# Performance work log

Hardware: AMD Instinct MI355X
Metric: run time of the kernel (lower is better)

## Reference

```python
import jax, jax.numpy as jnp
import numpy as np

EPS = 1e-8

def setup_inputs() -> dict:
    key = jax.random.key(0)
    kq, kk, kc, ks = jax.random.split(key, 4)
    d, m, K, Q, N = 128, 128, 4, 512, 131072
    query = jax.random.normal(kq, (Q, d), jnp.float32)
    keys = jax.random.normal(kk, (N, d), jnp.float32)
    # per-coordinate MSE codebook centers (sorted), scaled for unit-norm vectors in R^d
    codebook = jnp.sort(jax.random.normal(kc, (K,), jnp.float32)) / jnp.sqrt(jnp.float32(d))
    # QJL random projection matrix S: (m, d)
    S = jax.random.normal(ks, (m, d), jnp.float32)
    return {"query": query, "keys": keys, "codebook": codebook, "S": S}

def reference(query, keys, codebook, S):
    m = S.shape[0]
    # --- quantize(keys): Algorithm 2 ---
    vec_norm = jnp.linalg.norm(keys, axis=-1)                    # (N,)  ||x||
    x_norm = keys / (vec_norm[:, None] + EPS)                    # normalize
    # Stage 1: MSE codebook quantize (per-coordinate nearest center)
    idx = jnp.argmin(jnp.abs(x_norm[..., None] - codebook), axis=-1)  # (N, d)
    x_mse = codebook[idx]                                        # dequantize (gather)
    # residual
    r = x_norm - x_mse                                           # (N, d)
    r_norm = jnp.linalg.norm(r, axis=-1)                         # (N,)
    # Stage 2: QJL sign quantization of projected residual
    signs = jnp.where(r @ S.T >= 0, 1.0, -1.0).astype(keys.dtype)  # (N, m)
    # --- inner_product(query, compressed) ---
    term1 = query @ x_mse.T                                      # (Q, N)  <q, k_mse>
    Sq = query @ S.T                                             # (Q, m)
    scale = jnp.sqrt(jnp.pi / 2.0) / m
    term2 = (Sq @ signs.T) * (r_norm * scale)[None, :]           # QJL correction
    return (term1 + term2) * vec_norm[None, :]                   # rescale by ||k||
```

## Files before the change

kernel.cpp:

```cpp
#include <hip/hip_runtime.h>
#include <stdint.h>


typedef __attribute__((ext_vector_type(8))) short bf16x8;
typedef __attribute__((ext_vector_type(4))) float f32x4;

__device__ __forceinline__ uint16_t f2bf(float x) {
    uint32_t u = __builtin_bit_cast(uint32_t, x);
    uint32_t r = (u + 0x7fffu + ((u >> 16) & 1u)) >> 16;
    return (uint16_t)r;
}

__device__ __forceinline__ void load_lds16(const void* g, void* l) {
    __builtin_amdgcn_global_load_lds(
        (const __attribute__((address_space(1))) void*)g,
        (__attribute__((address_space(3))) void*)l, 16, 0, 0);
}

#define SLD 129

__global__ __launch_bounds__(256) void prep_keys(
    const float* __restrict__ keys, const float* __restrict__ codebook,
    const float* __restrict__ S, uint16_t* __restrict__ Bhat, int N)
{
    __shared__ float S_lds[128 * SLD];
    __shared__ float r_rm[16 * 132];
    __shared__ float rtmp[128];
    __shared__ float vn_sh[16];
    __shared__ float w_sh[16];

    const int tid = threadIdx.x;
    const int lane = tid & 63;
    const float c0 = codebook[0], c1 = codebook[1], c2 = codebook[2], c3 = codebook[3];
    const float scale = 0.009791516697777346f;

    for (int f = tid; f < 4096; f += 256) {
        float4 v = ((const float4*)S)[f];
        int j = f >> 5;
        int i0 = (f & 31) * 4;
        float* p = &S_lds[j * SLD + i0];
        p[0] = v.x; p[1] = v.y; p[2] = v.z; p[3] = v.w;
    }

    for (int tile = 0; tile < 16; ++tile) {
        const int n0 = blockIdx.x * 256 + tile * 16;
        __syncthreads();

        #pragma unroll
        for (int u = 0; u < 2; ++u) {
            int f = u * 256 + tid;
            int row = f >> 5;
            int i0 = (f & 31) * 4;
            float4 v = ((const float4*)(keys + (size_t)(n0 + row) * 128))[f & 31];
            *(float4*)&r_rm[row * 132 + i0] = v;
        }
        __syncthreads();

        if (tid < 128) {
            int row = tid >> 3, k = tid & 7;
            const float* x = &r_rm[row * 132];
            float a;
            {
                #pragma clang fp contract(off)
                float x0 = x[k];
                a = x0 * x0;
                for (int t = 1; t < 16; ++t) {
                    float xv = x[t * 8 + k];
                    a = a + xv * xv;
                }
            }
            rtmp[tid] = a;
        }
        __syncthreads();

        if (tid < 16) {
            const float* r = &rtmp[tid * 8];
            float res = ((r[0] + r[1]) + (r[2] + r[3])) + ((r[4] + r[5]) + (r[6] + r[7]));
            vn_sh[tid] = sqrtf(res);
        }
        __syncthreads();

        {
            int row = tid >> 4, i0 = (tid & 15) * 8;
            float vn = vn_sh[row];
            float denom = vn + 1e-8f;
            float rsq = 0.f;
            uint32_t pk[4];
            float rloc[8];
            #pragma unroll
            for (int u = 0; u < 8; ++u) {
                float xv = r_rm[row * 132 + i0 + u];
                float xn = xv / denom;
                float b = c0, d = fabsf(xn - c0), t;
                t = fabsf(xn - c1); if (t < d) { d = t; b = c1; }
                t = fabsf(xn - c2); if (t < d) { d = t; b = c2; }
                t = fabsf(xn - c3); if (t < d) { d = t; b = c3; }
                float rv = xn - b;
                rloc[u] = rv;
                rsq += rv * rv;
                uint32_t bv = f2bf(vn * b);
                if (u & 1) pk[u >> 1] |= bv << 16; else pk[u >> 1] = bv;
            }
            *(uint4*)(Bhat + (size_t)(n0 + row) * 256 + i0) = *(uint4*)pk;
            *(float4*)&r_rm[row * 132 + i0] = *(float4*)&rloc[0];
            *(float4*)&r_rm[row * 132 + i0 + 4] = *(float4*)&rloc[4];
            #pragma unroll
            for (int off2 = 1; off2 < 16; off2 <<= 1) rsq += __shfl_xor(rsq, off2);
            if ((tid & 15) == 0) w_sh[row] = sqrtf(rsq) * scale * vn;
        }
        __syncthreads();

        {
            const int rowgrp = tid >> 7;
            const int j = tid & 127;
            float rr[8][2];
            #pragma unroll
            for (int k = 0; k < 8; ++k) {
                rr[k][0] = r_rm[(rowgrp * 8 + k) * 132 + lane];
                rr[k][1] = r_rm[(rowgrp * 8 + k) * 132 + 64 + lane];
            }
            float acc[8] = {0.f, 0.f, 0.f, 0.f, 0.f, 0.f, 0.f, 0.f};
            const float* Sj = &S_lds[j * SLD];
            #pragma unroll
            for (int h = 0; h < 2; ++h) {
                #pragma unroll 8
                for (int i = 0; i < 64; ++i) {
                    float sv = Sj[h * 64 + i];
                    #pragma unroll
                    for (int k = 0; k < 8; ++k) {
                        int rb = __builtin_amdgcn_readlane(
                            __builtin_bit_cast(int, rr[k][h]), i);
                        acc[k] = __builtin_fmaf(__builtin_bit_cast(float, rb), sv, acc[k]);
                    }
                }
            }
            #pragma unroll
            for (int k = 0; k < 8; ++k) {
                float wv = w_sh[rowgrp * 8 + k];
                float v = (acc[k] >= 0.f) ? wv : -wv;
                Bhat[(size_t)(n0 + rowgrp * 8 + k) * 256 + 128 + j] = f2bf(v);
            }
        }
    }
}

__global__ __launch_bounds__(256) void prep_A(
    const float* __restrict__ query, const float* __restrict__ S,
    uint16_t* __restrict__ Ahat)
{
    int gid = blockIdx.x * 256 + threadIdx.x;
    int q = gid >> 7, j = gid & 127;
    const float4* qr = (const float4*)(query + (size_t)q * 128);
    const float4* sr = (const float4*)(S + (size_t)j * 128);
    float acc = 0.f;
    #pragma unroll
    for (int i = 0; i < 32; ++i) {
        float4 a = qr[i], b = sr[i];
        acc += a.x * b.x + a.y * b.y + a.z * b.z + a.w * b.w;
    }
    Ahat[(size_t)q * 256 + j] = f2bf(query[(size_t)q * 128 + j]);
    Ahat[(size_t)q * 256 + 128 + j] = f2bf(acc);
}

__global__ __launch_bounds__(256) void gemm_bt(
    const uint16_t* __restrict__ A, const uint16_t* __restrict__ B,
    float* __restrict__ C, int N, int Q)
{
    __shared__ uint16_t Asl[128 * 64];
    __shared__ uint16_t Bsl[128 * 64];
    const int tid = threadIdx.x;
    const int lane = tid & 63, wid = tid >> 6;

    const int nbn = N >> 7, nbm = Q >> 7;
    const int f = blockIdx.x;
    int bm_idx, bn_idx;
    if ((nbn & 7) == 0) {
        const int xcd = f & 7, s = f >> 3;
        const int pxb = nbn >> 3;
        const int sq = s / nbm;
        bn_idx = xcd * pxb + sq;
        bm_idx = s - sq * nbm;
    } else {
        bn_idx = f % nbn;
        bm_idx = f / nbn;
    }
    const int bm = bm_idx * 128;
    const int bn = bn_idx * 128;

    const int wm = (wid & 1) * 64, wn = (wid >> 1) * 64;
    const int lrow = lane & 15, lquad = lane >> 4;
    f32x4 acc[4][4] = {};

    #pragma unroll
    for (int kc = 0; kc < 256; kc += 64) {
        __syncthreads();
        #pragma unroll
        for (int u = 0; u < 4; ++u) {
            int flat = u * 256 + tid;
            int row = flat >> 3, ch = flat & 7;
            load_lds16(A + (size_t)(bm + row) * 256 + kc + ch * 8, &Asl[flat * 8]);
            load_lds16(B + (size_t)(bn + row) * 256 + kc + ch * 8, &Bsl[flat * 8]);
        }
        __syncthreads();
        #pragma unroll
        for (int ks = 0; ks < 2; ++ks) {
            bf16x8 af[4], bfr[4];
            #pragma unroll
            for (int ff = 0; ff < 4; ++ff) {
                af[ff]  = *(const bf16x8*)&Asl[(wm + ff * 16 + lrow) * 64 + ks * 32 + lquad * 8];
                bfr[ff] = *(const bf16x8*)&Bsl[(wn + ff * 16 + lrow) * 64 + ks * 32 + lquad * 8];
            }
            #pragma unroll
            for (int i = 0; i < 4; ++i)
                #pragma unroll
                for (int j = 0; j < 4; ++j)
                    acc[i][j] = __builtin_amdgcn_mfma_f32_16x16x32_bf16(af[i], bfr[j], acc[i][j], 0, 0, 0);
        }
    }

    #pragma unroll
    for (int i = 0; i < 4; ++i) {
        int row = bm + wm + i * 16 + lquad * 4;
        #pragma unroll
        for (int j = 0; j < 4; ++j) {
            int col = bn + wn + j * 16 + lrow;
            float* cp = C + (size_t)row * N + col;
            #pragma unroll
            for (int r = 0; r < 4; ++r) cp[(size_t)r * N] = acc[i][j][r];
        }
    }
}

extern "C" void kernel_launch(void* const* d_in, const int* in_sizes, int n_in,
                              void* d_out, int out_size, void* d_ws, size_t ws_size,
                              hipStream_t stream) {
    const float* query    = (const float*)d_in[0];
    const float* keys     = (const float*)d_in[1];
    const float* codebook = (const float*)d_in[2];
    const float* S        = (const float*)d_in[3];
    const int Q = in_sizes[0] / 128;
    const int N = in_sizes[1] / 128;

    uint16_t* Bhat = (uint16_t*)d_ws;
    uint16_t* Ahat = (uint16_t*)((char*)d_ws + (size_t)N * 256 * 2);

    prep_keys<<<N / 256, 256, 0, stream>>>(keys, codebook, S, Bhat, N);
    prep_A<<<(Q * 128) / 256, 256, 0, stream>>>(query, S, Ahat);
    gemm_bt<<<(N / 128) * (Q / 128), 256, 0, stream>>>(Ahat, Bhat, (float*)d_out, N, Q);
}
```

Baseline: 531.7 us.

## Split key prep into quantize and sign-projection kernels via scratch residuals

The residual projection and sign step moves out of prep_keys into a separate sign_dots kernel. prep_keys now writes residuals and per-row weights to scratch space borrowed from the output buffer. The old kernel needed a 66KB S tile in LDS plus readlane broadcasts, which limited occupancy and spent many instructions per FMA. The new kernel reads residuals as wave-uniform float4 loads from global memory, at the cost of an extra kernel launch and a round trip of about 64MB through memory.

```diff
diff --git a/kernel.cpp b/kernel.cpp
--- a/kernel.cpp
+++ b/kernel.cpp
@@ -17,30 +17,18 @@
         (__attribute__((address_space(3))) void*)l, 16, 0, 0);
 }
 
-#define SLD 129
-
 __global__ __launch_bounds__(256) void prep_keys(
     const float* __restrict__ keys, const float* __restrict__ codebook,
-    const float* __restrict__ S, uint16_t* __restrict__ Bhat, int N)
-{
-    __shared__ float S_lds[128 * SLD];
+    uint16_t* __restrict__ Bhat, float* __restrict__ rout,
+    float* __restrict__ wout, int N)
+{
     __shared__ float r_rm[16 * 132];
     __shared__ float rtmp[128];
     __shared__ float vn_sh[16];
-    __shared__ float w_sh[16];
 
     const int tid = threadIdx.x;
-    const int lane = tid & 63;
     const float c0 = codebook[0], c1 = codebook[1], c2 = codebook[2], c3 = codebook[3];
     const float scale = 0.009791516697777346f;
-
-    for (int f = tid; f < 4096; f += 256) {
-        float4 v = ((const float4*)S)[f];
-        int j = f >> 5;
-        int i0 = (f & 31) * 4;
-        float* p = &S_lds[j * SLD + i0];
-        p[0] = v.x; p[1] = v.y; p[2] = v.z; p[3] = v.w;
-    }
 
     for (int tile = 0; tile < 16; ++tile) {
         const int n0 = blockIdx.x * 256 + tile * 16;
@@ -102,44 +90,57 @@
                 if (u & 1) pk[u >> 1] |= bv << 16; else pk[u >> 1] = bv;
             }
             *(uint4*)(Bhat + (size_t)(n0 + row) * 256 + i0) = *(uint4*)pk;
-            *(float4*)&r_rm[row * 132 + i0] = *(float4*)&rloc[0];
-            *(float4*)&r_rm[row * 132 + i0 + 4] = *(float4*)&rloc[4];
+            float* rp = rout + (size_t)(n0 + row) * 128 + i0;
+            *(float4*)rp       = *(float4*)&rloc[0];
+            *(float4*)(rp + 4) = *(float4*)&rloc[4];
             #pragma unroll
             for (int off2 = 1; off2 < 16; off2 <<= 1) rsq += __shfl_xor(rsq, off2);
-            if ((tid & 15) == 0) w_sh[row] = sqrtf(rsq) * scale * vn;
-        }
-        __syncthreads();
-
-        {
-            const int rowgrp = tid >> 7;
-            const int j = tid & 127;
-            float rr[8][2];
+            if ((tid & 15) == 0) wout[n0 + row] = sqrtf(rsq) * scale * vn;
+        }
+    }
+}
+
+__global__ __launch_bounds__(256) void sign_dots(
+    const float* __restrict__ r, const float* __restrict__ w,
+    const float* __restrict__ S, uint16_t* __restrict__ Bhat, int N)
+{
+    __shared__ float S_lds[128 * 132];
+    const int tid = threadIdx.x;
+    const int lane = tid & 63;
+    const int wid = tid >> 6;
+
+    for (int f = tid; f < 4096; f += 256) {
+        float4 v = ((const float4*)S)[f];
+        int j = f >> 5, i0 = (f & 31) * 4;
+        *(float4*)&S_lds[j * 132 + i0] = v;
+    }
+    __syncthreads();
+
+    const int j = ((wid & 1) << 6) | lane;
+    const float* Sj = &S_lds[j * 132];
+    const int rowsel = (wid >> 1) * 8;
+
+    for (int tile = 0; tile < 16; ++tile) {
+        const int n0 = blockIdx.x * 256 + tile * 16 + rowsel;
+        const float* rb = r + (size_t)n0 * 128;
+        float acc[8] = {0.f, 0.f, 0.f, 0.f, 0.f, 0.f, 0.f, 0.f};
+        #pragma unroll 4
+        for (int i0 = 0; i0 < 128; i0 += 4) {
+            float4 sv = *(const float4*)(Sj + i0);
             #pragma unroll
             for (int k = 0; k < 8; ++k) {
-                rr[k][0] = r_rm[(rowgrp * 8 + k) * 132 + lane];
-                rr[k][1] = r_rm[(rowgrp * 8 + k) * 132 + 64 + lane];
-            }
-            float acc[8] = {0.f, 0.f, 0.f, 0.f, 0.f, 0.f, 0.f, 0.f};
-            const float* Sj = &S_lds[j * SLD];
-            #pragma unroll
-            for (int h = 0; h < 2; ++h) {
-                #pragma unroll 8
-                for (int i = 0; i < 64; ++i) {
-                    float sv = Sj[h * 64 + i];
-                    #pragma unroll
-                    for (int k = 0; k < 8; ++k) {
-                        int rb = __builtin_amdgcn_readlane(
-                            __builtin_bit_cast(int, rr[k][h]), i);
-                        acc[k] = __builtin_fmaf(__builtin_bit_cast(float, rb), sv, acc[k]);
-                    }
-                }
-            }
-            #pragma unroll
-            for (int k = 0; k < 8; ++k) {
-                float wv = w_sh[rowgrp * 8 + k];
-                float v = (acc[k] >= 0.f) ? wv : -wv;
-                Bhat[(size_t)(n0 + rowgrp * 8 + k) * 256 + 128 + j] = f2bf(v);
-            }
+                float4 rv = *(const float4*)(rb + k * 128 + i0);
+                acc[k] = __builtin_fmaf(rv.x, sv.x, acc[k]);
+                acc[k] = __builtin_fmaf(rv.y, sv.y, acc[k]);
+                acc[k] = __builtin_fmaf(rv.z, sv.z, acc[k]);
+                acc[k] = __builtin_fmaf(rv.w, sv.w, acc[k]);
+            }
+        }
+        #pragma unroll
+        for (int k = 0; k < 8; ++k) {
+            float wv = w[n0 + k];
+            float v = (acc[k] >= 0.f) ? wv : -wv;
+            Bhat[(size_t)(n0 + k) * 256 + 128 + j] = f2bf(v);
         }
     }
 }
@@ -213,8 +214,8 @@
             #pragma unroll
             for (int i = 0; i < 4; ++i)
                 #pragma unroll
-                for (int j = 0; j < 4; ++j)
-                    acc[i][j] = __builtin_amdgcn_mfma_f32_16x16x32_bf16(af[i], bfr[j], acc[i][j], 0, 0, 0);
+                for (int jj = 0; jj < 4; ++jj)
+                    acc[i][jj] = __builtin_amdgcn_mfma_f32_16x16x32_bf16(af[i], bfr[jj], acc[i][jj], 0, 0, 0);
         }
     }
 
@@ -222,11 +223,11 @@
     for (int i = 0; i < 4; ++i) {
         int row = bm + wm + i * 16 + lquad * 4;
         #pragma unroll
-        for (int j = 0; j < 4; ++j) {
-            int col = bn + wn + j * 16 + lrow;
+        for (int jj = 0; jj < 4; ++jj) {
+            int col = bn + wn + jj * 16 + lrow;
             float* cp = C + (size_t)row * N + col;
             #pragma unroll
-            for (int r = 0; r < 4; ++r) cp[(size_t)r * N] = acc[i][j][r];
+            for (int rr = 0; rr < 4; ++rr) cp[(size_t)rr * N] = acc[i][jj][rr];
         }
     }
 }
@@ -244,7 +245,11 @@
     uint16_t* Bhat = (uint16_t*)d_ws;
     uint16_t* Ahat = (uint16_t*)((char*)d_ws + (size_t)N * 256 * 2);
 
-    prep_keys<<<N / 256, 256, 0, stream>>>(keys, codebook, S, Bhat, N);
+    float* r_ws = (float*)d_out;
+    float* w_ws = (float*)d_out + (size_t)N * 128;
+
+    prep_keys<<<N / 256, 256, 0, stream>>>(keys, codebook, Bhat, r_ws, w_ws, N);
+    sign_dots<<<N / 256, 256, 0, stream>>>(r_ws, w_ws, S, Bhat, N);
     prep_A<<<(Q * 128) / 256, 256, 0, stream>>>(query, S, Ahat);
     gemm_bt<<<(N / 128) * (Q / 128), 256, 0, stream>>>(Ahat, Bhat, (float*)d_out, N, Q);
 }
```

After: 624.5 us. 1.17x slower.
